# Kernel optimization log

Hardware: AMD Instinct MI355X
Metric: run time of the kernel (lower is better)

The kernel has to match this reference:

```python
import jax, jax.numpy as jnp
import numpy as np

B, N, S, C, NS = 2, 20000, 1024, 256, 16
RADIUS, HMIN, HMAX = 0.05, -0.02, 0.04
NA, ND = 12, 4
EPS = 1e-5  # BatchNorm eps


def setup_inputs() -> dict:
    key = jax.random.key(0)
    ks = jax.random.split(key, 40)
    def rn(k, shape, scale=0.05):
        return jax.random.normal(k, shape, jnp.float32) * scale
    inp = {
        "xyz": jax.random.uniform(ks[0], (B, N, 3), jnp.float32),
        "new_xyz": jax.random.uniform(ks[1], (B, S, 3), jnp.float32),
        "view_rot": jax.random.normal(ks[2], (B, S, 3, 3), jnp.float32),
        "features": jax.random.normal(ks[3], (B, C, N), jnp.float32),
    }
    i = 4
    for li, (o, ci) in enumerate([(512, C + 3), (256, 512), (256, 256)], 1):
        inp[f"mlp{li}_w"] = rn(ks[i], (o, ci)); inp[f"mlp{li}_b"] = rn(ks[i + 1], (o,))
        inp[f"mlp{li}_g"] = jnp.ones((o,), jnp.float32) + rn(ks[i + 2], (o,), 0.01)
        inp[f"mlp{li}_be"] = rn(ks[i + 3], (o,)); i += 4
    for name in ("c1", "c2"):
        inp[f"{name}_w"] = rn(ks[i], (256, 256)); inp[f"{name}_b"] = rn(ks[i + 1], (256,))
        inp[f"{name}_g"] = jnp.ones((256,), jnp.float32) + rn(ks[i + 2], (256,), 0.01)
        inp[f"{name}_be"] = rn(ks[i + 3], (256,)); i += 4
    inp["c3_w"] = rn(ks[i], (NA * ND * 2, 256)); inp["c3_b"] = rn(ks[i + 1], (NA * ND * 2,))
    return inp


def _bn(x, g, be):  # eval-mode BatchNorm with running_mean=0, running_var=1
    return x * (g / jnp.sqrt(1.0 + EPS)) + be


def _forward(xyz, new_xyz, view_rot, features,
             mlp1_w, mlp1_b, mlp1_g, mlp1_be,
             mlp2_w, mlp2_b, mlp2_g, mlp2_be,
             mlp3_w, mlp3_b, mlp3_g, mlp3_be,
             c1_w, c1_b, c1_g, c1_be,
             c2_w, c2_b, c2_g, c2_be,
             c3_w, c3_b):
    # ---- cylinder query (CUDA kernel math: r = rot @ (p - c), cylinder axis = x) ----
    # computed per rotation row to keep intermediates at (B,S,N) each
    comp = []
    for i in range(3):
        rw = view_rot[:, :, i, :]  # (B,S,3)
        comp.append(jnp.einsum('bsj,bpj->bsp', rw, xyz) - jnp.sum(rw * new_xyz, -1)[..., None])
    xr, yr, zr = comp  # each (B,S,N)
    mask = (yr * yr + zr * zr < RADIUS * RADIUS) & (xr > HMIN) & (xr < HMAX)
    # first-NS valid indices per seed (ascending), pad with first valid (0 if none)
    vals = jnp.where(mask, jnp.arange(N, dtype=jnp.int32), N)  # (B,S,N)
    neg_top, _ = jax.lax.top_k(-vals, NS)
    idx = -neg_top  # (B,S,NS) ascending
    first = idx[..., :1]
    first = jnp.where(first >= N, 0, first)
    idx = jnp.where(idx >= N, first, idx)
    # ---- group ----
    b_ix = jnp.arange(B)[:, None, None]
    g_xyz = xyz[b_ix, idx]                                  # (B,S,NS,3)
    g_feat = jnp.transpose(features, (0, 2, 1))[b_ix, idx]  # (B,S,NS,C)
    diff = (g_xyz - new_xyz[:, :, None, :]) / RADIUS        # normalize_xyz
    rot_xyz = jnp.einsum('bsnk,bskj->bsnj', diff, view_rot)  # rotate_xyz: diff @ rot
    h = jnp.concatenate([rot_xyz, g_feat], axis=-1)          # (B,S,NS,C+3)
    # ---- SharedMLP (1x1 conv2d + BN + ReLU) ----
    for w, bb, g, be in ((mlp1_w, mlp1_b, mlp1_g, mlp1_be),
                         (mlp2_w, mlp2_b, mlp2_g, mlp2_be),
                         (mlp3_w, mlp3_b, mlp3_g, mlp3_be)):
        h = jax.nn.relu(_bn(jnp.einsum('bsnc,oc->bsno', h, w) + bb, g, be))
    h = h.max(axis=2)  # max-pool over samples -> (B,S,256)
    # ---- pointwise conv1d head ----
    h = jax.nn.relu(_bn(jnp.einsum('bsc,oc->bso', h, c1_w) + c1_b, c1_g, c1_be))
    h = jax.nn.relu(_bn(jnp.einsum('bsc,oc->bso', h, c2_w) + c2_b, c2_g, c2_be))
    out = jnp.einsum('bsc,oc->bso', h, c3_w) + c3_b  # (B,S,NA*ND*2)
    return out


def reference(xyz, new_xyz, view_rot, features,
              mlp1_w, mlp1_b, mlp1_g, mlp1_be,
              mlp2_w, mlp2_b, mlp2_g, mlp2_be,
              mlp3_w, mlp3_b, mlp3_g, mlp3_be,
              c1_w, c1_b, c1_g, c1_be,
              c2_w, c2_b, c2_g, c2_be,
              c3_w, c3_b):
    return _forward(xyz, new_xyz, view_rot, features,
                    mlp1_w, mlp1_b, mlp1_g, mlp1_be,
                    mlp2_w, mlp2_b, mlp2_g, mlp2_be,
                    mlp3_w, mlp3_b, mlp3_g, mlp3_be,
                    c1_w, c1_b, c1_g, c1_be,
                    c2_w, c2_b, c2_g, c2_be,
                    c3_w, c3_b)
```

## Files before the change

kernel.cpp:

```cpp
#include <hip/hip_runtime.h>
#include <hip/hip_bf16.h>
#include <stdint.h>

#define B_   2
#define N_   20000
#define S_   1024
#define C_   256
#define NS_  16
#define NQ   (B_ * S_)
#define M_   (NQ * NS_)
#define K1P  288
#define O1   512
#define O2   256
#define O3   256
#define OUTC 96

#define R2C   ((float)(0.05 * 0.05))
#define HMINC ((float)(-0.02))
#define HMAXC ((float)(0.04))

__device__ __forceinline__ unsigned short f2b(float f) {
    union { float f; unsigned int i; } x; x.f = f;
    unsigned int r = x.i + 0x7FFFu + ((x.i >> 16) & 1u);
    return (unsigned short)(r >> 16);
}
__device__ __forceinline__ float b2f(unsigned short u) {
    union { unsigned int i; float f; } x; x.i = ((unsigned int)u) << 16; return x.f;
}

__global__ __launch_bounds__(256) void prep_w123(const float* __restrict__ m1w,
                                                 const float* __restrict__ m2w,
                                                 const float* __restrict__ m3w,
                                                 unsigned short* __restrict__ w1p,
                                                 unsigned short* __restrict__ w2p,
                                                 unsigned short* __restrict__ w3p) {
    int i = blockIdx.x * 256 + threadIdx.x;
    if (i < O1 * K1P) {
        int o = i / K1P, k = i - o * K1P;
        float v = 0.0f;
        if (k < 256)      v = m1w[o * 259 + 3 + k];
        else if (k < 259) v = m1w[o * 259 + (k - 256)];
        w1p[i] = (k < 259) ? f2b(v) : (unsigned short)0;
    } else if (i < O1 * K1P + O2 * 512) {
        int j = i - O1 * K1P;
        w2p[j] = f2b(m2w[j]);
    } else if (i < O1 * K1P + O2 * 512 + O3 * 256) {
        int j = i - O1 * K1P - O2 * 512;
        w3p[j] = f2b(m3w[j]);
    }
}

__global__ __launch_bounds__(256) void prep_head_w(const float* __restrict__ c1w,
                                                   const float* __restrict__ c2w,
                                                   const float* __restrict__ c3w,
                                                   unsigned short* __restrict__ c1wb,
                                                   unsigned short* __restrict__ c2wb,
                                                   unsigned short* __restrict__ c3wb) {
    int i = blockIdx.x * 256 + threadIdx.x;
    if (i < 65536) {
        c1wb[i] = f2b(c1w[i]);
    } else if (i < 131072) {
        c2wb[i - 65536] = f2b(c2w[i - 65536]);
    } else if (i < 163840) {
        int j = i - 131072;
        int o = j >> 8, k = j & 255;
        c3wb[j] = (o < OUTC) ? f2b(c3w[o * 256 + k]) : (unsigned short)0;
    }
}

__global__ __launch_bounds__(256) void transpose_feat(const float* __restrict__ feat,
                                                      unsigned short* __restrict__ feat_t) {
    __shared__ float tile[32][33];
    int n0 = blockIdx.x * 32, c0 = blockIdx.y * 32, b = blockIdx.z;
    int t = threadIdx.x;
    int nl = t & 31;
#pragma unroll
    for (int i = 0; i < 4; ++i) {
        int cl = (t >> 5) + i * 8;
        tile[cl][nl] = feat[((size_t)(b * C_ + c0 + cl)) * N_ + n0 + nl];
    }
    __syncthreads();
    int nr = t >> 3, c4 = (t & 7) * 4;
    ushort4 v;
    v.x = f2b(tile[c4 + 0][nr]);
    v.y = f2b(tile[c4 + 1][nr]);
    v.z = f2b(tile[c4 + 2][nr]);
    v.w = f2b(tile[c4 + 3][nr]);
    *(ushort4*)(feat_t + ((size_t)(b * N_ + n0 + nr)) * C_ + c0 + c4) = v;
}

__global__ __launch_bounds__(256) void cyl_query(const float* __restrict__ xyz,
                                                 const float* __restrict__ new_xyz,
                                                 const float* __restrict__ view_rot,
                                                 int* __restrict__ idx_out) {
#pragma clang fp contract(off)
    int q = blockIdx.x;
    int b = q >> 10;
    int t = threadIdx.x;
    int w = t >> 6, lane = t & 63;

    __shared__ int lists[4][NS_];
    __shared__ int cnts[4];

    const float* nq = new_xyz + (size_t)q * 3;
    float qx = nq[0], qy = nq[1], qz = nq[2];
    const float* rp = view_rot + (size_t)q * 9;
    float R[9];
#pragma unroll
    for (int i = 0; i < 9; ++i) R[i] = rp[i];
    float dq0 = (R[0]*qx + R[1]*qy) + R[2]*qz;
    float dq1 = (R[3]*qx + R[4]*qy) + R[5]*qz;
    float dq2 = (R[6]*qx + R[7]*qy) + R[8]*qz;

    int start = w * 5000;
    int end   = min(N_, start + 5000);
    int cnt = 0;
    const float* xb = xyz + (size_t)b * N_ * 3;

    for (int base = start; base < end && cnt < NS_; base += 64) {
        int p = base + lane;
        bool m = false;
        if (p < end) {
            const float* pp = xb + (size_t)p * 3;
            float px = pp[0], py = pp[1], pz = pp[2];
            float xr = ((R[0]*px + R[1]*py) + R[2]*pz) - dq0;
            float yr = ((R[3]*px + R[4]*py) + R[5]*pz) - dq1;
            float zr = ((R[6]*px + R[7]*py) + R[8]*pz) - dq2;
            m = ((yr*yr + zr*zr) < R2C) && (xr > HMINC) && (xr < HMAXC);
        }
        unsigned long long bal = __ballot(m);
        int below = __popcll(bal & ((1ull << lane) - 1ull));
        if (m) {
            int pos = cnt + below;
            if (pos < NS_) lists[w][pos] = p;
        }
        cnt += (int)__popcll(bal);
        if (cnt > NS_) cnt = NS_;
    }
    if (lane == 0) cnts[w] = cnt;
    __syncthreads();

    if (t == 0) {
        int buf[NS_]; int total = 0;
        for (int ww = 0; ww < 4 && total < NS_; ++ww)
            for (int i = 0; i < cnts[ww] && total < NS_; ++i)
                buf[total++] = lists[ww][i];
        int first = (total > 0) ? buf[0] : 0;
        for (int i = 0; i < NS_; ++i)
            idx_out[q * NS_ + i] = (i < total) ? buf[i] : first;
    }
}

__global__ __launch_bounds__(256) void build_h0(const float* __restrict__ xyz,
                                                const float* __restrict__ new_xyz,
                                                const float* __restrict__ view_rot,
                                                const unsigned short* __restrict__ feat_t,
                                                const int* __restrict__ idxs,
                                                unsigned short* __restrict__ h0) {
#pragma clang fp contract(off)
    int q = blockIdx.x;
    int b = q >> 10;
    int t = threadIdx.x;
    __shared__ int pidx[NS_];
    if (t < NS_) pidx[t] = idxs[q * NS_ + t];
    __syncthreads();

#pragma unroll
    for (int pass = 0; pass < 2; ++pass) {
        int n = pass * 8 + (t >> 5);
        int p = pidx[n];
        uint4 v = *(const uint4*)(feat_t + ((size_t)(b * N_ + p)) * C_ + (t & 31) * 8);
        *(uint4*)(h0 + (size_t)(q * NS_ + n) * K1P + (t & 31) * 8) = v;
    }

    if (t < NS_) {
        int n = t, p = pidx[n];
        const float* pp = xyz + ((size_t)b * N_ + p) * 3;
        const float* nq = new_xyz + (size_t)q * 3;
        float dx = (pp[0] - nq[0]) / 0.05f;
        float dy = (pp[1] - nq[1]) / 0.05f;
        float dz = (pp[2] - nq[2]) / 0.05f;
        const float* rp = view_rot + (size_t)q * 9;
        float r0 = (dx * rp[0] + dy * rp[3]) + dz * rp[6];
        float r1 = (dx * rp[1] + dy * rp[4]) + dz * rp[7];
        float r2 = (dx * rp[2] + dy * rp[5]) + dz * rp[8];
        size_t row = (size_t)(q * NS_ + n) * K1P;
        h0[row + 256] = f2b(r0);
        h0[row + 257] = f2b(r1);
        h0[row + 258] = f2b(r2);
    }
    for (int e = t; e < NS_ * 29; e += 256) {
        int n = e / 29, c = 259 + (e - n * 29);
        h0[(size_t)(q * NS_ + n) * K1P + c] = 0;
    }
}

typedef float f32x4 __attribute__((ext_vector_type(4)));
typedef short s16x8 __attribute__((ext_vector_type(8)));

__global__ __launch_bounds__(256) void gemm_bn_relu(const unsigned short* __restrict__ A,
                                                    const unsigned short* __restrict__ W,
                                                    const float* __restrict__ bias,
                                                    const float* __restrict__ gam,
                                                    const float* __restrict__ bet,
                                                    unsigned short* __restrict__ out,
                                                    int M, int Nn, int K) {
    __shared__ __align__(16) unsigned short As[128 * 32];
    __shared__ __align__(16) unsigned short Bs[128 * 32];
    int tid  = threadIdx.x;
    int lane = tid & 63, wave = tid >> 6;
    int m0 = blockIdx.x * 128, n0 = blockIdx.y * 128;
    int wm = (wave >> 1) * 64, wn = (wave & 1) * 64;

    f32x4 acc[4][4] = {};

    for (int k0 = 0; k0 < K; k0 += 32) {
        __syncthreads();
#pragma unroll
        for (int j = 0; j < 2; ++j) {
            int e = j * 256 + tid;
            int r = e >> 2, c8 = (e & 3) << 3;
            *(uint4*)&As[e * 8] = *(const uint4*)(A + (size_t)(m0 + r) * K + k0 + c8);
            *(uint4*)&Bs[e * 8] = *(const uint4*)(W + (size_t)(n0 + r) * K + k0 + c8);
        }
        __syncthreads();

        int kq = (lane >> 4) * 8, rr = lane & 15;
        s16x8 af[4], bfr[4];
#pragma unroll
        for (int i = 0; i < 4; ++i) af[i]  = *(const s16x8*)&As[(wm + i * 16 + rr) * 32 + kq];
#pragma unroll
        for (int j = 0; j < 4; ++j) bfr[j] = *(const s16x8*)&Bs[(wn + j * 16 + rr) * 32 + kq];
#pragma unroll
        for (int i = 0; i < 4; ++i)
#pragma unroll
            for (int j = 0; j < 4; ++j)
                acc[i][j] = __builtin_amdgcn_mfma_f32_16x16x32_bf16(af[i], bfr[j], acc[i][j], 0, 0, 0);
    }

    float inv = 1.0f / sqrtf(1.0f + 1e-5f);
    int col = lane & 15, rq = (lane >> 4) * 4;
#pragma unroll
    for (int j = 0; j < 4; ++j) {
        int n = n0 + wn + j * 16 + col;
        float sc = gam[n] * inv;
        float tb = bias[n] * sc + bet[n];
#pragma unroll
        for (int i = 0; i < 4; ++i) {
            int mbase = m0 + wm + i * 16 + rq;
#pragma unroll
            for (int r = 0; r < 4; ++r) {
                float v = acc[i][j][r] * sc + tb;
                v = fmaxf(v, 0.0f);
                out[(size_t)(mbase + r) * Nn + n] = f2b(v);
            }
        }
    }
}

__global__ __launch_bounds__(256) void gemm_bn_relu_maxpool(const unsigned short* __restrict__ A,
                                                            const unsigned short* __restrict__ W,
                                                            const float* __restrict__ bias,
                                                            const float* __restrict__ gam,
                                                            const float* __restrict__ bet,
                                                            unsigned short* __restrict__ hp,
                                                            int M, int Nn, int K) {
    __shared__ __align__(16) unsigned short As[128 * 32];
    __shared__ __align__(16) unsigned short Bs[128 * 32];
    int tid  = threadIdx.x;
    int lane = tid & 63, wave = tid >> 6;
    int m0 = blockIdx.x * 128, n0 = blockIdx.y * 128;
    int wm = (wave >> 1) * 64, wn = (wave & 1) * 64;

    f32x4 acc[4][4] = {};

    for (int k0 = 0; k0 < K; k0 += 32) {
        __syncthreads();
#pragma unroll
        for (int j = 0; j < 2; ++j) {
            int e = j * 256 + tid;
            int r = e >> 2, c8 = (e & 3) << 3;
            *(uint4*)&As[e * 8] = *(const uint4*)(A + (size_t)(m0 + r) * K + k0 + c8);
            *(uint4*)&Bs[e * 8] = *(const uint4*)(W + (size_t)(n0 + r) * K + k0 + c8);
        }
        __syncthreads();

        int kq = (lane >> 4) * 8, rr = lane & 15;
        s16x8 af[4], bfr[4];
#pragma unroll
        for (int i = 0; i < 4; ++i) af[i]  = *(const s16x8*)&As[(wm + i * 16 + rr) * 32 + kq];
#pragma unroll
        for (int j = 0; j < 4; ++j) bfr[j] = *(const s16x8*)&Bs[(wn + j * 16 + rr) * 32 + kq];
#pragma unroll
        for (int i = 0; i < 4; ++i)
#pragma unroll
            for (int j = 0; j < 4; ++j)
                acc[i][j] = __builtin_amdgcn_mfma_f32_16x16x32_bf16(af[i], bfr[j], acc[i][j], 0, 0, 0);
    }

    float inv = 1.0f / sqrtf(1.0f + 1e-5f);
    int col = lane & 15;
    int qbase = (m0 + wm) >> 4;
#pragma unroll
    for (int j = 0; j < 4; ++j) {
        int n = n0 + wn + j * 16 + col;
        float sc = gam[n] * inv;
        float tb = bias[n] * sc + bet[n];
#pragma unroll
        for (int i = 0; i < 4; ++i) {
            float mx = 0.0f;
#pragma unroll
            for (int r = 0; r < 4; ++r)
                mx = fmaxf(mx, acc[i][j][r] * sc + tb);
            mx = fmaxf(mx, __shfl_xor(mx, 16, 64));
            mx = fmaxf(mx, __shfl_xor(mx, 32, 64));
            if (lane < 16)
                hp[(size_t)(qbase + i) * Nn + n] = f2b(mx);
        }
    }
}

__global__ __launch_bounds__(256) void gemm_c3(const unsigned short* __restrict__ A,
                                               const unsigned short* __restrict__ W,
                                               const float* __restrict__ bias,
                                               float* __restrict__ out,
                                               int M, int K) {
    __shared__ __align__(16) unsigned short As[128 * 32];
    __shared__ __align__(16) unsigned short Bs[128 * 32];
    int tid  = threadIdx.x;
    int lane = tid & 63, wave = tid >> 6;
    int m0 = blockIdx.x * 128;
    int wm = (wave >> 1) * 64, wn = (wave & 1) * 64;

    f32x4 acc[4][4] = {};

    for (int k0 = 0; k0 < K; k0 += 32) {
        __syncthreads();
#pragma unroll
        for (int j = 0; j < 2; ++j) {
            int e = j * 256 + tid;
            int r = e >> 2, c8 = (e & 3) << 3;
            *(uint4*)&As[e * 8] = *(const uint4*)(A + (size_t)(m0 + r) * K + k0 + c8);
            *(uint4*)&Bs[e * 8] = *(const uint4*)(W + (size_t)r * K + k0 + c8);
        }
        __syncthreads();

        int kq = (lane >> 4) * 8, rr = lane & 15;
        s16x8 af[4], bfr[4];
#pragma unroll
        for (int i = 0; i < 4; ++i) af[i]  = *(const s16x8*)&As[(wm + i * 16 + rr) * 32 + kq];
#pragma unroll
        for (int j = 0; j < 4; ++j) bfr[j] = *(const s16x8*)&Bs[(wn + j * 16 + rr) * 32 + kq];
#pragma unroll
        for (int i = 0; i < 4; ++i)
#pragma unroll
            for (int j = 0; j < 4; ++j)
                acc[i][j] = __builtin_amdgcn_mfma_f32_16x16x32_bf16(af[i], bfr[j], acc[i][j], 0, 0, 0);
    }

    int col = lane & 15, rq = (lane >> 4) * 4;
#pragma unroll
    for (int j = 0; j < 4; ++j) {
        int n = wn + j * 16 + col;
        if (n >= OUTC) continue;
        float bb = bias[n];
#pragma unroll
        for (int i = 0; i < 4; ++i) {
            int mbase = m0 + wm + i * 16 + rq;
#pragma unroll
            for (int r = 0; r < 4; ++r)
                out[(size_t)(mbase + r) * OUTC + n] = acc[i][j][r] + bb;
        }
    }
}

extern "C" void kernel_launch(void* const* d_in, const int* in_sizes, int n_in,
                              void* d_out, int out_size, void* d_ws, size_t ws_size,
                              hipStream_t stream) {
    const float* xyz      = (const float*)d_in[0];
    const float* new_xyz  = (const float*)d_in[1];
    const float* view_rot = (const float*)d_in[2];
    const float* feat     = (const float*)d_in[3];
    const float* m1w = (const float*)d_in[4];
    const float* m1b = (const float*)d_in[5];
    const float* m1g = (const float*)d_in[6];
    const float* m1be= (const float*)d_in[7];
    const float* m2w = (const float*)d_in[8];
    const float* m2b = (const float*)d_in[9];
    const float* m2g = (const float*)d_in[10];
    const float* m2be= (const float*)d_in[11];
    const float* m3w = (const float*)d_in[12];
    const float* m3b = (const float*)d_in[13];
    const float* m3g = (const float*)d_in[14];
    const float* m3be= (const float*)d_in[15];
    const float* c1w = (const float*)d_in[16];
    const float* c1b = (const float*)d_in[17];
    const float* c1g = (const float*)d_in[18];
    const float* c1be= (const float*)d_in[19];
    const float* c2w = (const float*)d_in[20];
    const float* c2b = (const float*)d_in[21];
    const float* c2g = (const float*)d_in[22];
    const float* c2be= (const float*)d_in[23];
    const float* c3w = (const float*)d_in[24];
    const float* c3b = (const float*)d_in[25];

    char* ws = (char*)d_ws;
    int*            idxs = (int*)ws;
    unsigned short* w1p  = (unsigned short*)(ws + 131072);
    unsigned short* w2p  = (unsigned short*)(ws + 425984);
    unsigned short* w3p  = (unsigned short*)(ws + 688128);
    unsigned short* h0   = (unsigned short*)(ws + 819200);
    char*           h1b  = ws + 19693568;
    unsigned short* h1   = (unsigned short*)h1b;
    unsigned short* h2   = h0;
    unsigned short* featt= (unsigned short*)(h1b + 12582912);
    unsigned short* hp   = (unsigned short*)(h1b + 0);
    unsigned short* g1   = (unsigned short*)(h1b + 4194304);
    unsigned short* g2   = (unsigned short*)(h1b + 8388608);
    unsigned short* c1wb = (unsigned short*)(h1b + 12582912);
    unsigned short* c2wb = (unsigned short*)(h1b + 13631488);
    unsigned short* c3wb = (unsigned short*)(h1b + 14680064);

    hipLaunchKernelGGL(prep_w123, dim3((O1 * K1P + O2 * 512 + O3 * 256) / 256), dim3(256), 0, stream,
                       m1w, m2w, m3w, w1p, w2p, w3p);
    hipLaunchKernelGGL(cyl_query, dim3(NQ), dim3(256), 0, stream, xyz, new_xyz, view_rot, idxs);
    hipLaunchKernelGGL(transpose_feat, dim3(N_ / 32, C_ / 32, B_), dim3(256), 0, stream, feat, featt);
    hipLaunchKernelGGL(build_h0, dim3(NQ), dim3(256), 0, stream, xyz, new_xyz, view_rot, featt, idxs, h0);
    hipLaunchKernelGGL(gemm_bn_relu, dim3(M_ / 128, O1 / 128), dim3(256), 0, stream,
                       h0, w1p, m1b, m1g, m1be, h1, M_, O1, K1P);
    hipLaunchKernelGGL(gemm_bn_relu, dim3(M_ / 128, O2 / 128), dim3(256), 0, stream,
                       h1, w2p, m2b, m2g, m2be, h2, M_, O2, 512);
    hipLaunchKernelGGL(prep_head_w, dim3(163840 / 256), dim3(256), 0, stream,
                       c1w, c2w, c3w, c1wb, c2wb, c3wb);
    hipLaunchKernelGGL(gemm_bn_relu_maxpool, dim3(M_ / 128, O3 / 128), dim3(256), 0, stream,
                       h2, w3p, m3b, m3g, m3be, hp, M_, O3, 256);
    hipLaunchKernelGGL(gemm_bn_relu, dim3(NQ / 128, 256 / 128), dim3(256), 0, stream,
                       hp, c1wb, c1b, c1g, c1be, g1, NQ, 256, 256);
    hipLaunchKernelGGL(gemm_bn_relu, dim3(NQ / 128, 256 / 128), dim3(256), 0, stream,
                       g1, c2wb, c2b, c2g, c2be, g2, NQ, 256, 256);
    hipLaunchKernelGGL(gemm_c3, dim3(NQ / 128), dim3(256), 0, stream,
                       g2, c3wb, c3b, (float*)d_out, NQ, 256);
}
```

Measured before the change: 269.4 us.

## Replace brute-force cylinder query with uniform-grid binned neighbor search

Adds a kernel that bins each point into a 16^3 grid with per-cell atomic counters, zeroing the counters inside the weight-prep kernel. The query kernel inverts each view rotation to get a world-space bounding box of the cylinder and tests only points in the overlapping cells. It then rank-sorts the candidates so the first 16 indices stay in ascending order. This is meant to avoid scanning all 20000 points per query, which the old kernel usually did because few seeds find 16 neighbours. Non-orthonormal rotations can give large boxes, so there is a full-scan fallback when the box covers too many cells or too many hits are found.

```diff
diff --git a/kernel.cpp b/kernel.cpp
--- a/kernel.cpp
+++ b/kernel.cpp
@@ -14,6 +14,8 @@
 #define O2   256
 #define O3   256
 #define OUTC 96
+#define GRID 16
+#define CELLCAP 64
 
 #define R2C   ((float)(0.05 * 0.05))
 #define HMINC ((float)(-0.02))
@@ -28,12 +30,13 @@
     union { unsigned int i; float f; } x; x.i = ((unsigned int)u) << 16; return x.f;
 }
 
-__global__ __launch_bounds__(256) void prep_w123(const float* __restrict__ m1w,
-                                                 const float* __restrict__ m2w,
-                                                 const float* __restrict__ m3w,
-                                                 unsigned short* __restrict__ w1p,
-                                                 unsigned short* __restrict__ w2p,
-                                                 unsigned short* __restrict__ w3p) {
+__global__ __launch_bounds__(256) void prep_all(const float* __restrict__ m1w,
+                                                const float* __restrict__ m2w,
+                                                const float* __restrict__ m3w,
+                                                unsigned short* __restrict__ w1p,
+                                                unsigned short* __restrict__ w2p,
+                                                unsigned short* __restrict__ w3p,
+                                                int* __restrict__ counts) {
     int i = blockIdx.x * 256 + threadIdx.x;
     if (i < O1 * K1P) {
         int o = i / K1P, k = i - o * K1P;
@@ -41,12 +44,14 @@
         if (k < 256)      v = m1w[o * 259 + 3 + k];
         else if (k < 259) v = m1w[o * 259 + (k - 256)];
         w1p[i] = (k < 259) ? f2b(v) : (unsigned short)0;
-    } else if (i < O1 * K1P + O2 * 512) {
-        int j = i - O1 * K1P;
+    } else if (i < 278528) {
+        int j = i - 147456;
         w2p[j] = f2b(m2w[j]);
-    } else if (i < O1 * K1P + O2 * 512 + O3 * 256) {
-        int j = i - O1 * K1P - O2 * 512;
+    } else if (i < 344064) {
+        int j = i - 278528;
         w3p[j] = f2b(m3w[j]);
+    } else if (i < 344064 + 2 * GRID * GRID * GRID) {
+        counts[i - 344064] = 0;
     }
 }
 
@@ -68,6 +73,22 @@
     }
 }
 
+__global__ __launch_bounds__(256) void bin_points(const float* __restrict__ xyz,
+                                                  int* __restrict__ counts,
+                                                  int* __restrict__ binned) {
+    int i = blockIdx.x * 256 + threadIdx.x;
+    if (i >= B_ * N_) return;
+    int b = (i >= N_) ? 1 : 0;
+    int p = i - b * N_;
+    const float* pp = xyz + ((size_t)b * N_ + p) * 3;
+    int cx = min(GRID - 1, max(0, (int)(pp[0] * GRID)));
+    int cy = min(GRID - 1, max(0, (int)(pp[1] * GRID)));
+    int cz = min(GRID - 1, max(0, (int)(pp[2] * GRID)));
+    int cell = ((b * GRID + cx) * GRID + cy) * GRID + cz;
+    int pos = atomicAdd(&counts[cell], 1);
+    if (pos < CELLCAP) binned[cell * CELLCAP + pos] = p;
+}
+
 __global__ __launch_bounds__(256) void transpose_feat(const float* __restrict__ feat,
                                                       unsigned short* __restrict__ feat_t) {
     __shared__ float tile[32][33];
@@ -89,18 +110,19 @@
     *(ushort4*)(feat_t + ((size_t)(b * N_ + n0 + nr)) * C_ + c0 + c4) = v;
 }
 
-__global__ __launch_bounds__(256) void cyl_query(const float* __restrict__ xyz,
-                                                 const float* __restrict__ new_xyz,
-                                                 const float* __restrict__ view_rot,
-                                                 int* __restrict__ idx_out) {
+__global__ __launch_bounds__(64) void cyl_query_binned(const float* __restrict__ xyz,
+                                                       const float* __restrict__ new_xyz,
+                                                       const float* __restrict__ view_rot,
+                                                       const int* __restrict__ counts,
+                                                       const int* __restrict__ binned,
+                                                       int* __restrict__ idx_out) {
 #pragma clang fp contract(off)
     int q = blockIdx.x;
     int b = q >> 10;
-    int t = threadIdx.x;
-    int w = t >> 6, lane = t & 63;
-
-    __shared__ int lists[4][NS_];
-    __shared__ int cnts[4];
+    int lane = threadIdx.x;
+
+    __shared__ int pass[64];
+    __shared__ int firstv;
 
     const float* nq = new_xyz + (size_t)q * 3;
     float qx = nq[0], qy = nq[1], qz = nq[2];
@@ -112,43 +134,97 @@
     float dq1 = (R[3]*qx + R[4]*qy) + R[5]*qz;
     float dq2 = (R[6]*qx + R[7]*qy) + R[8]*qz;
 
-    int start = w * 5000;
-    int end   = min(N_, start + 5000);
+    float a00 = R[4]*R[8] - R[5]*R[7], a01 = R[2]*R[7] - R[1]*R[8], a02 = R[1]*R[5] - R[2]*R[4];
+    float a10 = R[5]*R[6] - R[3]*R[8], a11 = R[0]*R[8] - R[2]*R[6], a12 = R[2]*R[3] - R[0]*R[5];
+    float a20 = R[3]*R[7] - R[4]*R[6], a21 = R[1]*R[6] - R[0]*R[7], a22 = R[0]*R[4] - R[1]*R[3];
+    float det = R[0]*a00 + R[1]*a10 + R[2]*a20;
+    float inv = 1.0f / det;
+    float lo[3], hi[3];
+    const float rho = 0.05f + 1e-3f;
+    const float qc[3] = {qx, qy, qz};
+    const float ar[3][3] = {{a00,a01,a02},{a10,a11,a12},{a20,a21,a22}};
+#pragma unroll
+    for (int k = 0; k < 3; ++k) {
+        float c0 = ar[k][0] * inv, c1 = ar[k][1] * inv, c2 = ar[k][2] * inv;
+        float e0 = c0 * HMINC, e1 = c0 * HMAXC;
+        float rr = rho * sqrtf(c1 * c1 + c2 * c2);
+        float l = qc[k] + fminf(e0, e1) - rr - 1e-3f;
+        float h = qc[k] + fmaxf(e0, e1) + rr + 1e-3f;
+        if (!(l > -1e6f && h < 1e6f)) { l = 0.0f; h = 1.0f; }
+        lo[k] = l; hi[k] = h;
+    }
+    int cx0 = max(0, (int)floorf(lo[0] * GRID)), cx1 = min(GRID - 1, (int)floorf(hi[0] * GRID));
+    int cy0 = max(0, (int)floorf(lo[1] * GRID)), cy1 = min(GRID - 1, (int)floorf(hi[1] * GRID));
+    int cz0 = max(0, (int)floorf(lo[2] * GRID)), cz1 = min(GRID - 1, (int)floorf(hi[2] * GRID));
+
+    const float* xb = xyz + (size_t)b * N_ * 3;
     int cnt = 0;
-    const float* xb = xyz + (size_t)b * N_ * 3;
-
-    for (int base = start; base < end && cnt < NS_; base += 64) {
-        int p = base + lane;
-        bool m = false;
-        if (p < end) {
-            const float* pp = xb + (size_t)p * 3;
-            float px = pp[0], py = pp[1], pz = pp[2];
-            float xr = ((R[0]*px + R[1]*py) + R[2]*pz) - dq0;
-            float yr = ((R[3]*px + R[4]*py) + R[5]*pz) - dq1;
-            float zr = ((R[6]*px + R[7]*py) + R[8]*pz) - dq2;
-            m = ((yr*yr + zr*zr) < R2C) && (xr > HMINC) && (xr < HMAXC);
-        }
-        unsigned long long bal = __ballot(m);
-        int below = __popcll(bal & ((1ull << lane) - 1ull));
-        if (m) {
-            int pos = cnt + below;
-            if (pos < NS_) lists[w][pos] = p;
-        }
-        cnt += (int)__popcll(bal);
-        if (cnt > NS_) cnt = NS_;
-    }
-    if (lane == 0) cnts[w] = cnt;
+    unsigned long long below_mask = (1ull << lane) - 1ull;
+
+    int ncells = (cx1 - cx0 + 1) * (cy1 - cy0 + 1) * (cz1 - cz0 + 1);
+    bool fallback = (ncells > 200);
+
+    if (!fallback) {
+        for (int cx = cx0; cx <= cx1; ++cx)
+        for (int cy = cy0; cy <= cy1; ++cy)
+        for (int cz = cz0; cz <= cz1; ++cz) {
+            int cell = ((b * GRID + cx) * GRID + cy) * GRID + cz;
+            int len = counts[cell];
+            if (len > CELLCAP) len = CELLCAP;
+            bool m = false; int p = 0;
+            if (lane < len) {
+                p = binned[cell * CELLCAP + lane];
+                const float* pp = xb + (size_t)p * 3;
+                float px = pp[0], py = pp[1], pz = pp[2];
+                float xr = ((R[0]*px + R[1]*py) + R[2]*pz) - dq0;
+                float yr = ((R[3]*px + R[4]*py) + R[5]*pz) - dq1;
+                float zr = ((R[6]*px + R[7]*py) + R[8]*pz) - dq2;
+                m = ((yr*yr + zr*zr) < R2C) && (xr > HMINC) && (xr < HMAXC);
+            }
+            unsigned long long bal = __ballot(m);
+            if (bal) {
+                int pos = cnt + (int)__popcll(bal & below_mask);
+                if (m && pos < 64) pass[pos] = p;
+                cnt += (int)__popcll(bal);
+            }
+        }
+        if (cnt > 64) fallback = true;
+    }
+
+    if (fallback) {
+        cnt = 0;
+        for (int base = 0; base < N_ && cnt < NS_; base += 64) {
+            int p = base + lane;
+            bool m = false;
+            if (p < N_) {
+                const float* pp = xb + (size_t)p * 3;
+                float px = pp[0], py = pp[1], pz = pp[2];
+                float xr = ((R[0]*px + R[1]*py) + R[2]*pz) - dq0;
+                float yr = ((R[3]*px + R[4]*py) + R[5]*pz) - dq1;
+                float zr = ((R[6]*px + R[7]*py) + R[8]*pz) - dq2;
+                m = ((yr*yr + zr*zr) < R2C) && (xr > HMINC) && (xr < HMAXC);
+            }
+            unsigned long long bal = __ballot(m);
+            int pos = cnt + (int)__popcll(bal & below_mask);
+            if (m && pos < NS_) pass[pos] = p;
+            cnt += (int)__popcll(bal);
+            if (cnt > NS_) cnt = NS_;
+        }
+    }
     __syncthreads();
 
-    if (t == 0) {
-        int buf[NS_]; int total = 0;
-        for (int ww = 0; ww < 4 && total < NS_; ++ww)
-            for (int i = 0; i < cnts[ww] && total < NS_; ++i)
-                buf[total++] = lists[ww][i];
-        int first = (total > 0) ? buf[0] : 0;
-        for (int i = 0; i < NS_; ++i)
-            idx_out[q * NS_ + i] = (i < total) ? buf[i] : first;
-    }
+    int cl = min(cnt, 64);
+    int v = 0x7fffffff;
+    if (lane < cl) v = pass[lane];
+    int rank = 0;
+    for (int j = 0; j < cl; ++j) rank += (pass[j] < v) ? 1 : 0;
+    if (lane == 0) firstv = 0;
+    __syncthreads();
+    if (lane < cl && rank == 0) firstv = v;
+    __syncthreads();
+    int first = firstv;
+    if (lane < cl && rank < 16) idx_out[q * NS_ + rank] = v;
+    if (lane >= cl && lane < 16) idx_out[q * NS_ + lane] = first;
 }
 
 __global__ __launch_bounds__(256) void build_h0(const float* __restrict__ xyz,
@@ -413,6 +489,8 @@
     char*           h1b  = ws + 19693568;
     unsigned short* h1   = (unsigned short*)h1b;
     unsigned short* h2   = h0;
+    int*            counts = (int*)(h1b + 0);
+    int*            binned = (int*)(h1b + 65536);
     unsigned short* featt= (unsigned short*)(h1b + 12582912);
     unsigned short* hp   = (unsigned short*)(h1b + 0);
     unsigned short* g1   = (unsigned short*)(h1b + 4194304);
@@ -421,9 +499,12 @@
     unsigned short* c2wb = (unsigned short*)(h1b + 13631488);
     unsigned short* c3wb = (unsigned short*)(h1b + 14680064);
 
-    hipLaunchKernelGGL(prep_w123, dim3((O1 * K1P + O2 * 512 + O3 * 256) / 256), dim3(256), 0, stream,
-                       m1w, m2w, m3w, w1p, w2p, w3p);
-    hipLaunchKernelGGL(cyl_query, dim3(NQ), dim3(256), 0, stream, xyz, new_xyz, view_rot, idxs);
+    hipLaunchKernelGGL(prep_all, dim3((344064 + 8192 + 255) / 256), dim3(256), 0, stream,
+                       m1w, m2w, m3w, w1p, w2p, w3p, counts);
+    hipLaunchKernelGGL(bin_points, dim3((B_ * N_ + 255) / 256), dim3(256), 0, stream,
+                       xyz, counts, binned);
+    hipLaunchKernelGGL(cyl_query_binned, dim3(NQ), dim3(64), 0, stream,
+                       xyz, new_xyz, view_rot, counts, binned, idxs);
     hipLaunchKernelGGL(transpose_feat, dim3(N_ / 32, C_ / 32, B_), dim3(256), 0, stream, feat, featt);
     hipLaunchKernelGGL(build_h0, dim3(NQ), dim3(256), 0, stream, xyz, new_xyz, view_rot, featt, idxs, h0);
     hipLaunchKernelGGL(gemm_bn_relu, dim3(M_ / 128, O1 / 128), dim3(256), 0, stream,
```

Measured after the change: 334.5 us. +24.2%, slower.
